# Kernel tuning notes

Measured on AMD Instinct MI355X. Metric: run time of the kernel, lower is better.

The kernel has to match this reference:

```python
import jax, jax.numpy as jnp
import numpy as np

TOKENS, IN_F, OUT_F = 8192, 4096, 4096
MAXQ = 15          # 4-bit
ZERO_POINT = 8     # (maxq + 1) // 2


def _make_24_mask(key, in_f, out_f):
    """Boolean 2:4 mask: exactly 2 True per contiguous group of 4 along in_f."""
    scores = jax.random.normal(key, (in_f // 4, 4, out_f), dtype=jnp.float32)
    # ascending sort along the group-of-4 axis; index 2 = 2nd largest value
    thresh = jnp.sort(scores, axis=1)[:, 2:3, :]
    mask = scores >= thresh  # keeps top-2 of each group of 4
    return mask.reshape(in_f, out_f)


def setup_inputs() -> dict:
    key = jax.random.key(0)
    k_x, k_q, k_m, k_s = jax.random.split(key, 4)
    x = jax.random.normal(k_x, (TOKENS, IN_F), dtype=jnp.float16)
    qvals = jax.random.randint(k_q, (IN_F, OUT_F), 0, MAXQ + 1, dtype=jnp.int32)
    mask = _make_24_mask(k_m, IN_F, OUT_F)
    # per-column scales (groupsize == infeatures -> one scale row)
    scales = (jax.random.uniform(k_s, (1, OUT_F), dtype=jnp.float32) * 0.01 + 0.001).astype(jnp.float16)
    return {"x": x, "qvals": qvals, "mask": mask, "scales": scales}


def reference(x, qvals, mask, scales):
    # Dequantize: W = (q - zero_point) * scale, then apply 2:4 sparsity mask.
    w = (qvals.astype(jnp.float32) - ZERO_POINT) * scales.astype(jnp.float32)  # [in, out]
    w = jnp.where(mask, w, 0.0).astype(x.dtype)
    # GEMM with fp32 accumulation (as the fused kernel does), output in x.dtype
    y = jnp.einsum("ti,io->to", x, w, preferred_element_type=jnp.float32)
    return y.astype(x.dtype)
```

## Files before the change

### kernel.cpp

```cpp
#include <hip/hip_runtime.h>
#include <stdint.h>

typedef short short8 __attribute__((ext_vector_type(8)));
typedef float floatx4 __attribute__((ext_vector_type(4)));

#define M_TOK 8192
#define K_IN  4096
#define N_OUT 4096
#define NTT   (K_IN / 32)

static __device__ __forceinline__ float bf2f(ushort u) {
    union { uint32_t u; float f; } v;
    v.u = ((uint32_t)u) << 16;
    return v.f;
}
static __device__ __forceinline__ ushort f2bf(float f) {
    union { float f; uint32_t u; } v;
    v.f = f;
    uint32_t u = v.u;
    uint32_t r = (u + 0x7FFFu + ((u >> 16) & 1u)) >> 16;
    return (ushort)r;
}

__global__ __launch_bounds__(256) void detect_kernel(
    const unsigned char* __restrict__ mb, int* __restrict__ flags) {
    const ushort* mh = (const ushort*)mb;
    const unsigned int* mw = (const unsigned int*)mb;
    __shared__ int v[3];
    if (threadIdx.x < 3) v[threadIdx.x] = 0;
    __syncthreads();
    int l0 = 0, l1 = 0, l2 = 0;
    for (int o = threadIdx.x; o < 4096; o += 256) {
        int c1 = 0, c2 = 0, c4 = 0;
        #pragma unroll
        for (int r = 0; r < 4; ++r) {
            int idx = r * N_OUT + o;
            c1 += (mb[idx] != 0);
            c2 += (mh[idx] != 0);
            c4 += (mw[idx] != 0);
        }
        l0 += (c1 != 2); l1 += (c2 != 2); l2 += (c4 != 2);
    }
    atomicAdd(&v[0], l0); atomicAdd(&v[1], l1); atomicAdd(&v[2], l2);
    __syncthreads();
    if (threadIdx.x == 0) {
        int size = 4, best = v[2];
        if (v[1] < best) { size = 2; best = v[1]; }
        if (v[0] < best) { size = 1; }
        flags[0] = size;
    }
}

__global__ __launch_bounds__(256) void prep_kernel(
    const float* __restrict__ xf, ushort* __restrict__ Xb,
    const int* __restrict__ q, const void* __restrict__ maskp,
    const float* __restrict__ scales, ushort* __restrict__ Bt,
    const int* __restrict__ flagp) {
    const int tid = threadIdx.x;
    if (blockIdx.x < 4096) {
        const int total = M_TOK * K_IN;
        const int stride = 4096 * 256 * 8;
        for (int i = (blockIdx.x * 256 + tid) * 8; i < total; i += stride) {
            floatx4 f0 = *(const floatx4*)&xf[i];
            floatx4 f1 = *(const floatx4*)&xf[i + 4];
            short8 v;
            #pragma unroll
            for (int j = 0; j < 4; ++j) v[j]     = (short)f2bf(f0[j]);
            #pragma unroll
            for (int j = 0; j < 4; ++j) v[4 + j] = (short)f2bf(f1[j]);
            *(short8*)&Xb[i] = v;
        }
    } else {
        const int d  = blockIdx.x - 4096;
        const int i0 = (d & 63) * 64;
        const int o0 = (d >> 6) * 64;
        const int msize = flagp[0];
        const unsigned char* mb = (const unsigned char*)maskp;
        const ushort* mh = (const ushort*)maskp;
        const unsigned int* mi = (const unsigned int*)maskp;
        __shared__ ushort T[64][72];
        for (int p = 0; p < 16; ++p) {
            int idx = p * 256 + tid;
            int r = idx >> 6, c = idx & 63;
            size_t gi = (size_t)(i0 + r) * N_OUT + (o0 + c);
            bool m;
            if (msize == 1)      m = (mb[gi] != 0);
            else if (msize == 2) m = (mh[gi] != 0);
            else                 m = (mi[gi] != 0);
            float s = scales[o0 + c];
            float w = m ? (float)(q[gi] - 8) * s : 0.0f;
            T[r][c] = f2bf(w);
        }
        __syncthreads();
        for (int p = 0; p < 2; ++p) {
            int ol = p * 32 + (tid >> 3);
            int i8 = (tid & 7) * 8;
            short8 v;
            #pragma unroll
            for (int j = 0; j < 8; ++j) v[j] = (short)T[i8 + j][ol];
            *(short8*)&Bt[(size_t)(o0 + ol) * K_IN + i0 + i8] = v;
        }
    }
}

#define GL2L16(gp, lbase)                                                      \
    __builtin_amdgcn_global_load_lds(                                          \
        (const __attribute__((address_space(1))) void*)(gp),                   \
        (__attribute__((address_space(3))) void*)(lbase), 16, 0, 0)

#define MFMA16(a, b, c) __builtin_amdgcn_mfma_f32_16x16x32_bf16(a, b, c, 0, 0, 0)

__global__ __launch_bounds__(256, 2) void gemm_kernel(
    const ushort* __restrict__ X,
    const ushort* __restrict__ Bt,
    float* __restrict__ Y) {
    __shared__ ushort As[3][128][32];
    __shared__ ushort Bs[3][256][32];

    const int tid  = threadIdx.x;
    const int w    = tid >> 6;
    const int lane = tid & 63;

    const int xcd = blockIdx.x & 7;
    const int jj  = (blockIdx.x >> 3) & 63;
    const int rr0 = blockIdx.x >> 9;
    const int m_tile = rr0 * 32 + (xcd & 1) * 16 + (jj & 15);
    const int n_tile = (xcd >> 1) * 4 + (jj >> 4);
    const int row0 = m_tile * 128;
    const int col0 = n_tile * 256;

    floatx4 acc[8][4] = {};

    const int schunk = (tid & 3) ^ ((tid >> 3) & 3);
    const ushort* gA = X  + (size_t)(row0 + (tid >> 2)) * K_IN + schunk * 8;
    const ushort* gB = Bt + (size_t)(col0 + (tid >> 2)) * K_IN + schunk * 8;

    const int fr = lane & 15, g = lane >> 4;
    const int fsw = (fr >> 1) & 3;

    #define STG(SL, tt)                                                        \
        do {                                                                   \
            GL2L16(gA + (size_t)(tt) * 32,                                     \
                   (char*)&As[SL][w * 16][0] + lane * 16);                     \
            GL2L16(gA + (size_t)64 * K_IN + (size_t)(tt) * 32,                 \
                   (char*)&As[SL][64 + w * 16][0] + lane * 16);                \
            GL2L16(gB + (size_t)(tt) * 32,                                     \
                   (char*)&Bs[SL][w * 16][0] + lane * 16);                     \
            GL2L16(gB + (size_t)64 * K_IN + (size_t)(tt) * 32,                 \
                   (char*)&Bs[SL][64 + w * 16][0] + lane * 16);                \
            GL2L16(gB + (size_t)128 * K_IN + (size_t)(tt) * 32,                \
                   (char*)&Bs[SL][128 + w * 16][0] + lane * 16);               \
            GL2L16(gB + (size_t)192 * K_IN + (size_t)(tt) * 32,                \
                   (char*)&Bs[SL][192 + w * 16][0] + lane * 16);               \
        } while (0)

    #define TILE(SL, T, SG, GATE_KIND)                                         \
        do {                                                                   \
            short8 afr[8], bfr[4];                                             \
            _Pragma("unroll")                                                  \
            for (int n = 0; n < 4; ++n)                                        \
                bfr[n] = *(const short8*)&Bs[SL][w * 64 + n * 16 + fr]         \
                             [(g ^ fsw) * 8];                                  \
            _Pragma("unroll")                                                  \
            for (int m = 0; m < 8; ++m)                                        \
                afr[m] = *(const short8*)&As[SL][m * 16 + fr][(g ^ fsw) * 8];  \
            if (SG) STG(((SL) + 2) % 3, (T) + 2);                              \
            __builtin_amdgcn_s_setprio(1);                                     \
            _Pragma("unroll")                                                  \
            for (int m = 0; m < 8; ++m)                                        \
                _Pragma("unroll")                                              \
                for (int n = 0; n < 4; ++n)                                    \
                    acc[m][n] = MFMA16(afr[m], bfr[n], acc[m][n]);             \
            __builtin_amdgcn_s_setprio(0);                                     \
            asm volatile("s_waitcnt lgkmcnt(0)" ::: "memory");                 \
            if ((GATE_KIND) == 0) {                                            \
                asm volatile("s_waitcnt vmcnt(6)" ::: "memory");               \
            } else if ((GATE_KIND) == 1) {                                     \
                asm volatile("s_waitcnt vmcnt(0)" ::: "memory");               \
            }                                                                  \
            if ((GATE_KIND) != 2) {                                            \
                __builtin_amdgcn_s_barrier();                                  \
                __builtin_amdgcn_sched_barrier(0);                             \
            }                                                                  \
        } while (0)

    STG(0, 0);
    STG(1, 1);
    asm volatile("s_waitcnt vmcnt(6)" ::: "memory");
    __builtin_amdgcn_s_barrier();
    __builtin_amdgcn_sched_barrier(0);

    for (int t = 0; t < 126; t += 3) {
        TILE(0, t,     true, 0);
        TILE(1, t + 1, true, 0);
        TILE(2, t + 2, true, 0);
    }
    TILE(0, 126, false, 1);
    TILE(1, 127, false, 2);

    const int fq = lane >> 4;
    #pragma unroll
    for (int m = 0; m < 8; ++m)
        #pragma unroll
        for (int n = 0; n < 4; ++n)
            #pragma unroll
            for (int i = 0; i < 4; ++i) {
                int rr = row0 + m * 16 + fq * 4 + i;
                int cc = col0 + w * 64 + n * 16 + fr;
                Y[(size_t)rr * N_OUT + cc] = acc[m][n][i];
            }
    #undef TILE
    #undef STG
}

__global__ __launch_bounds__(256) void fallback_kernel(
    const float* __restrict__ xf, const int* __restrict__ q,
    const void* __restrict__ maskp, const float* __restrict__ scales,
    float* __restrict__ Y, const int* __restrict__ flagp) {
    const int msize = flagp[0];
    const int o = blockIdx.x * 256 + threadIdx.x;
    const int t = blockIdx.y;
    const unsigned char* mb = (const unsigned char*)maskp;
    const ushort* mh = (const ushort*)maskp;
    const unsigned int* mi = (const unsigned int*)maskp;
    float s = scales[o];
    float acc = 0.f;
    for (int i = 0; i < K_IN; ++i) {
        float x = bf2f(f2bf(xf[(size_t)t * K_IN + i]));
        size_t gi = (size_t)i * N_OUT + o;
        bool m;
        if (msize == 1)      m = (mb[gi] != 0);
        else if (msize == 2) m = (mh[gi] != 0);
        else                 m = (mi[gi] != 0);
        if (m) acc += x * bf2f(f2bf((float)(q[gi] - 8) * s));
    }
    Y[(size_t)t * N_OUT + o] = acc;
}

extern "C" void kernel_launch(void* const* d_in, const int* in_sizes, int n_in,
                              void* d_out, int out_size, void* d_ws, size_t ws_size,
                              hipStream_t stream) {
    const float* x      = (const float*)d_in[0];
    const int*   q      = (const int*)d_in[1];
    const void*  mask   = d_in[2];
    const float* scales = (const float*)d_in[3];
    float* y = (float*)d_out;

    const size_t BT_OFF = 64;
    const size_t XB_OFF = BT_OFF + (size_t)N_OUT * K_IN * 2;
    const size_t need   = XB_OFF + (size_t)M_TOK * K_IN * 2;

    int* flags = (int*)d_ws;
    detect_kernel<<<1, 256, 0, stream>>>((const unsigned char*)mask, flags);

    if (ws_size >= need) {
        ushort* Bt = (ushort*)((char*)d_ws + BT_OFF);
        ushort* Xb = (ushort*)((char*)d_ws + XB_OFF);
        prep_kernel<<<8192, 256, 0, stream>>>(x, Xb, q, mask, scales, Bt, flags);
        gemm_kernel<<<dim3((M_TOK / 128) * (N_OUT / 256)), 256, 0, stream>>>(
            Xb, Bt, y);
    } else {
        fallback_kernel<<<dim3(N_OUT / 256, M_TOK), 256, 0, stream>>>(
            x, q, mask, scales, y, flags);
    }
}
```

Measured before the change: 360.2 us.

## Switch GEMM to 32x32x16 MFMA with double-buffered LDS pipeline

Replaces the 16x16x32 bf16 MFMA tiling with 32x32x16 MFMAs, which cuts the number of LDS fragment reads per output and the instruction count per k-step. It also drops the three-stage LDS ring with partial vmcnt gating for a simpler two-buffer scheme that prefetches one tile ahead and waits for all loads before each barrier. The larger MFMA shape may raise throughput, but the shallower prefetch and the full vmcnt(0) wait every iteration expose more global-load latency.

```diff
diff --git a/kernel.cpp b/kernel.cpp
--- a/kernel.cpp
+++ b/kernel.cpp
@@ -3,6 +3,7 @@
 
 typedef short short8 __attribute__((ext_vector_type(8)));
 typedef float floatx4 __attribute__((ext_vector_type(4)));
+typedef float floatx16 __attribute__((ext_vector_type(16)));
 
 #define M_TOK 8192
 #define K_IN  4096
@@ -108,14 +109,14 @@
         (const __attribute__((address_space(1))) void*)(gp),                   \
         (__attribute__((address_space(3))) void*)(lbase), 16, 0, 0)
 
-#define MFMA16(a, b, c) __builtin_amdgcn_mfma_f32_16x16x32_bf16(a, b, c, 0, 0, 0)
+#define MFMA32(a, b, c) __builtin_amdgcn_mfma_f32_32x32x16_bf16(a, b, c, 0, 0, 0)
 
 __global__ __launch_bounds__(256, 2) void gemm_kernel(
     const ushort* __restrict__ X,
     const ushort* __restrict__ Bt,
     float* __restrict__ Y) {
-    __shared__ ushort As[3][128][32];
-    __shared__ ushort Bs[3][256][32];
+    __shared__ ushort As[2][128][32];
+    __shared__ ushort Bs[2][256][32];
 
     const int tid  = threadIdx.x;
     const int w    = tid >> 6;
@@ -129,85 +130,87 @@
     const int row0 = m_tile * 128;
     const int col0 = n_tile * 256;
 
-    floatx4 acc[8][4] = {};
+    floatx16 acc[4][2] = {};
 
     const int schunk = (tid & 3) ^ ((tid >> 3) & 3);
     const ushort* gA = X  + (size_t)(row0 + (tid >> 2)) * K_IN + schunk * 8;
     const ushort* gB = Bt + (size_t)(col0 + (tid >> 2)) * K_IN + schunk * 8;
 
-    const int fr = lane & 15, g = lane >> 4;
-    const int fsw = (fr >> 1) & 3;
-
-    #define STG(SL, tt)                                                        \
+    const int r32 = lane & 31, hi = lane >> 5;
+    const int fsw = (r32 >> 1) & 3;
+
+    #define STG(BF, tt)                                                        \
         do {                                                                   \
             GL2L16(gA + (size_t)(tt) * 32,                                     \
-                   (char*)&As[SL][w * 16][0] + lane * 16);                     \
+                   (char*)&As[BF][w * 16][0] + lane * 16);                     \
             GL2L16(gA + (size_t)64 * K_IN + (size_t)(tt) * 32,                 \
-                   (char*)&As[SL][64 + w * 16][0] + lane * 16);                \
+                   (char*)&As[BF][64 + w * 16][0] + lane * 16);                \
             GL2L16(gB + (size_t)(tt) * 32,                                     \
-                   (char*)&Bs[SL][w * 16][0] + lane * 16);                     \
+                   (char*)&Bs[BF][w * 16][0] + lane * 16);                     \
             GL2L16(gB + (size_t)64 * K_IN + (size_t)(tt) * 32,                 \
-                   (char*)&Bs[SL][64 + w * 16][0] + lane * 16);                \
+                   (char*)&Bs[BF][64 + w * 16][0] + lane * 16);                \
             GL2L16(gB + (size_t)128 * K_IN + (size_t)(tt) * 32,                \
-                   (char*)&Bs[SL][128 + w * 16][0] + lane * 16);               \
+                   (char*)&Bs[BF][128 + w * 16][0] + lane * 16);               \
             GL2L16(gB + (size_t)192 * K_IN + (size_t)(tt) * 32,                \
-                   (char*)&Bs[SL][192 + w * 16][0] + lane * 16);               \
+                   (char*)&Bs[BF][192 + w * 16][0] + lane * 16);               \
         } while (0)
 
-    #define TILE(SL, T, SG, GATE_KIND)                                         \
+    #define TILE(BF, T)                                                        \
         do {                                                                   \
-            short8 afr[8], bfr[4];                                             \
-            _Pragma("unroll")                                                  \
-            for (int n = 0; n < 4; ++n)                                        \
-                bfr[n] = *(const short8*)&Bs[SL][w * 64 + n * 16 + fr]         \
-                             [(g ^ fsw) * 8];                                  \
-            _Pragma("unroll")                                                  \
-            for (int m = 0; m < 8; ++m)                                        \
-                afr[m] = *(const short8*)&As[SL][m * 16 + fr][(g ^ fsw) * 8];  \
-            if (SG) STG(((SL) + 2) % 3, (T) + 2);                              \
+            short8 a0[4], a1[4], b0[2], b1[2];                                 \
+            _Pragma("unroll")                                                  \
+            for (int nb = 0; nb < 2; ++nb) {                                   \
+                b0[nb] = *(const short8*)&Bs[BF][w * 64 + nb * 32 + r32]       \
+                             [((0 + hi) ^ fsw) * 8];                           \
+                b1[nb] = *(const short8*)&Bs[BF][w * 64 + nb * 32 + r32]       \
+                             [((2 + hi) ^ fsw) * 8];                           \
+            }                                                                  \
+            _Pragma("unroll")                                                  \
+            for (int mb = 0; mb < 4; ++mb) {                                   \
+                a0[mb] = *(const short8*)&As[BF][mb * 32 + r32]                \
+                             [((0 + hi) ^ fsw) * 8];                           \
+                a1[mb] = *(const short8*)&As[BF][mb * 32 + r32]                \
+                             [((2 + hi) ^ fsw) * 8];                           \
+            }                                                                  \
+            if ((T) + 1 < NTT) STG((BF) ^ 1, (T) + 1);                         \
+            __builtin_amdgcn_s_barrier();                                      \
+            asm volatile("s_waitcnt lgkmcnt(0)" ::: "memory");                 \
+            __builtin_amdgcn_sched_barrier(0);                                 \
             __builtin_amdgcn_s_setprio(1);                                     \
             _Pragma("unroll")                                                  \
-            for (int m = 0; m < 8; ++m)                                        \
+            for (int mb = 0; mb < 4; ++mb)                                     \
                 _Pragma("unroll")                                              \
-                for (int n = 0; n < 4; ++n)                                    \
-                    acc[m][n] = MFMA16(afr[m], bfr[n], acc[m][n]);             \
+                for (int nb = 0; nb < 2; ++nb)                                 \
+                    acc[mb][nb] = MFMA32(a0[mb], b0[nb], acc[mb][nb]);         \
+            _Pragma("unroll")                                                  \
+            for (int mb = 0; mb < 4; ++mb)                                     \
+                _Pragma("unroll")                                              \
+                for (int nb = 0; nb < 2; ++nb)                                 \
+                    acc[mb][nb] = MFMA32(a1[mb], b1[nb], acc[mb][nb]);         \
             __builtin_amdgcn_s_setprio(0);                                     \
-            asm volatile("s_waitcnt lgkmcnt(0)" ::: "memory");                 \
-            if ((GATE_KIND) == 0) {                                            \
-                asm volatile("s_waitcnt vmcnt(6)" ::: "memory");               \
-            } else if ((GATE_KIND) == 1) {                                     \
-                asm volatile("s_waitcnt vmcnt(0)" ::: "memory");               \
-            }                                                                  \
-            if ((GATE_KIND) != 2) {                                            \
-                __builtin_amdgcn_s_barrier();                                  \
-                __builtin_amdgcn_sched_barrier(0);                             \
-            }                                                                  \
+            asm volatile("s_waitcnt vmcnt(0)" ::: "memory");                   \
+            __builtin_amdgcn_s_barrier();                                      \
         } while (0)
 
     STG(0, 0);
-    STG(1, 1);
-    asm volatile("s_waitcnt vmcnt(6)" ::: "memory");
+    asm volatile("s_waitcnt vmcnt(0)" ::: "memory");
     __builtin_amdgcn_s_barrier();
-    __builtin_amdgcn_sched_barrier(0);
-
-    for (int t = 0; t < 126; t += 3) {
-        TILE(0, t,     true, 0);
-        TILE(1, t + 1, true, 0);
-        TILE(2, t + 2, true, 0);
-    }
-    TILE(0, 126, false, 1);
-    TILE(1, 127, false, 2);
-
-    const int fq = lane >> 4;
+
+    for (int t = 0; t < NTT; t += 2) {
+        TILE(0, t);
+        TILE(1, t + 1);
+    }
+
     #pragma unroll
-    for (int m = 0; m < 8; ++m)
+    for (int mb = 0; mb < 4; ++mb)
         #pragma unroll
-        for (int n = 0; n < 4; ++n)
-            #pragma unroll
-            for (int i = 0; i < 4; ++i) {
-                int rr = row0 + m * 16 + fq * 4 + i;
-                int cc = col0 + w * 64 + n * 16 + fr;
-                Y[(size_t)rr * N_OUT + cc] = acc[m][n][i];
+        for (int nb = 0; nb < 2; ++nb)
+            #pragma unroll
+            for (int reg = 0; reg < 16; ++reg) {
+                int crow = (reg & 3) + 8 * (reg >> 2) + 4 * hi;
+                int rr = row0 + mb * 32 + crow;
+                int cc = col0 + w * 64 + nb * 32 + r32;
+                Y[(size_t)rr * N_OUT + cc] = acc[mb][nb][reg];
             }
     #undef TILE
     #undef STG
```

After: 391.3 us. 1.09x slower.

## Switch GEMM to double-buffered LDS pipeline with staggered block start

Applied to the files above, without the earlier changes.

Replaces the three-stage LDS ring (prefetch two tiles ahead) with a two-stage double buffer that prefetches one tile ahead and adds an extra barrier per tile. Odd blocks sleep briefly at start to stagger memory traffic between co-resident blocks. The smaller LDS footprint could improve occupancy, but prefetch distance drops and each tile now waits for all loads (vmcnt(0)), so memory latency is hidden less.

```diff
diff --git a/kernel.cpp b/kernel.cpp
--- a/kernel.cpp
+++ b/kernel.cpp
@@ -114,12 +114,14 @@
     const ushort* __restrict__ X,
     const ushort* __restrict__ Bt,
     float* __restrict__ Y) {
-    __shared__ ushort As[3][128][32];
-    __shared__ ushort Bs[3][256][32];
+    __shared__ ushort As[2][128][32];
+    __shared__ ushort Bs[2][256][32];
 
     const int tid  = threadIdx.x;
     const int w    = tid >> 6;
     const int lane = tid & 63;
+
+    if (blockIdx.x & 1) __builtin_amdgcn_s_sleep(10);
 
     const int xcd = blockIdx.x & 7;
     const int jj  = (blockIdx.x >> 3) & 63;
@@ -138,33 +140,36 @@
     const int fr = lane & 15, g = lane >> 4;
     const int fsw = (fr >> 1) & 3;
 
-    #define STG(SL, tt)                                                        \
+    #define STG(BF, tt)                                                        \
         do {                                                                   \
             GL2L16(gA + (size_t)(tt) * 32,                                     \
-                   (char*)&As[SL][w * 16][0] + lane * 16);                     \
+                   (char*)&As[BF][w * 16][0] + lane * 16);                     \
             GL2L16(gA + (size_t)64 * K_IN + (size_t)(tt) * 32,                 \
-                   (char*)&As[SL][64 + w * 16][0] + lane * 16);                \
+                   (char*)&As[BF][64 + w * 16][0] + lane * 16);                \
             GL2L16(gB + (size_t)(tt) * 32,                                     \
-                   (char*)&Bs[SL][w * 16][0] + lane * 16);                     \
+                   (char*)&Bs[BF][w * 16][0] + lane * 16);                     \
             GL2L16(gB + (size_t)64 * K_IN + (size_t)(tt) * 32,                 \
-                   (char*)&Bs[SL][64 + w * 16][0] + lane * 16);                \
+                   (char*)&Bs[BF][64 + w * 16][0] + lane * 16);                \
             GL2L16(gB + (size_t)128 * K_IN + (size_t)(tt) * 32,                \
-                   (char*)&Bs[SL][128 + w * 16][0] + lane * 16);               \
+                   (char*)&Bs[BF][128 + w * 16][0] + lane * 16);               \
             GL2L16(gB + (size_t)192 * K_IN + (size_t)(tt) * 32,                \
-                   (char*)&Bs[SL][192 + w * 16][0] + lane * 16);               \
+                   (char*)&Bs[BF][192 + w * 16][0] + lane * 16);               \
         } while (0)
 
-    #define TILE(SL, T, SG, GATE_KIND)                                         \
+    #define TILE(BF, T)                                                        \
         do {                                                                   \
             short8 afr[8], bfr[4];                                             \
             _Pragma("unroll")                                                  \
             for (int n = 0; n < 4; ++n)                                        \
-                bfr[n] = *(const short8*)&Bs[SL][w * 64 + n * 16 + fr]         \
+                bfr[n] = *(const short8*)&Bs[BF][w * 64 + n * 16 + fr]         \
                              [(g ^ fsw) * 8];                                  \
             _Pragma("unroll")                                                  \
             for (int m = 0; m < 8; ++m)                                        \
-                afr[m] = *(const short8*)&As[SL][m * 16 + fr][(g ^ fsw) * 8];  \
-            if (SG) STG(((SL) + 2) % 3, (T) + 2);                              \
+                afr[m] = *(const short8*)&As[BF][m * 16 + fr][(g ^ fsw) * 8];  \
+            if ((T) + 1 < NTT) STG((BF) ^ 1, (T) + 1);                         \
+            __builtin_amdgcn_s_barrier();                                      \
+            asm volatile("s_waitcnt lgkmcnt(0)" ::: "memory");                 \
+            __builtin_amdgcn_sched_barrier(0);                                 \
             __builtin_amdgcn_s_setprio(1);                                     \
             _Pragma("unroll")                                                  \
             for (int m = 0; m < 8; ++m)                                        \
@@ -172,31 +177,18 @@
                 for (int n = 0; n < 4; ++n)                                    \
                     acc[m][n] = MFMA16(afr[m], bfr[n], acc[m][n]);             \
             __builtin_amdgcn_s_setprio(0);                                     \
-            asm volatile("s_waitcnt lgkmcnt(0)" ::: "memory");                 \
-            if ((GATE_KIND) == 0) {                                            \
-                asm volatile("s_waitcnt vmcnt(6)" ::: "memory");               \
-            } else if ((GATE_KIND) == 1) {                                     \
-                asm volatile("s_waitcnt vmcnt(0)" ::: "memory");               \
-            }                                                                  \
-            if ((GATE_KIND) != 2) {                                            \
-                __builtin_amdgcn_s_barrier();                                  \
-                __builtin_amdgcn_sched_barrier(0);                             \
-            }                                                                  \
+            asm volatile("s_waitcnt vmcnt(0)" ::: "memory");                   \
+            __builtin_amdgcn_s_barrier();                                      \
         } while (0)
 
     STG(0, 0);
-    STG(1, 1);
-    asm volatile("s_waitcnt vmcnt(6)" ::: "memory");
+    asm volatile("s_waitcnt vmcnt(0)" ::: "memory");
     __builtin_amdgcn_s_barrier();
-    __builtin_amdgcn_sched_barrier(0);
-
-    for (int t = 0; t < 126; t += 3) {
-        TILE(0, t,     true, 0);
-        TILE(1, t + 1, true, 0);
-        TILE(2, t + 2, true, 0);
-    }
-    TILE(0, 126, false, 1);
-    TILE(1, 127, false, 2);
+
+    for (int t = 0; t < NTT; t += 2) {
+        TILE(0, t);
+        TILE(1, t + 1);
+    }
 
     const int fq = lane >> 4;
     #pragma unroll
```

After: 360.2 us. Within noise of the previous version (-0.0%).
